# Performance work log

Measured on AMD Instinct MI355X. Metric: run time of the kernel, lower is better.

Reference implementation:

```python
import jax, jax.numpy as jnp
import numpy as np

MASK_VALUE = 0.0  # default `mask=0` scalar in the original forward


def setup_inputs() -> dict:
    key = jax.random.key(0)
    kq, kk, kv = jax.random.split(key, 3)
    b, n, d_k, d_v = 8, 2048, 64, 64
    q = jax.random.normal(kq, (b, n, d_k), dtype=jnp.float32)
    k = jax.random.normal(kk, (b, n, d_k), dtype=jnp.float32)
    v = jax.random.normal(kv, (b, n, d_v), dtype=jnp.float32)
    return {"q": q, "k": k, "v": v}


def reference(q, k, v):
    d_k = q.shape[-1]
    temper = jnp.asarray(d_k, q.dtype) ** 0.5
    # scores: (b, n, n)
    attn = jnp.einsum('bqd,bkd->bqk', q, k) / temper
    # equality-based masking: positions whose score exactly equals the
    # scalar `mask` (default 0) are set to -inf before softmax.
    attn = jnp.where(attn == MASK_VALUE, -jnp.inf, attn)
    # NOTE: the original code calls `attn.masked_fill(look_ahead_mask==0, -inf)`
    # WITHOUT assignment, so the look-ahead mask is a no-op; we omit it faithfully.
    attn = jax.nn.softmax(attn, axis=-1)
    out = jnp.einsum('bqk,bkd->bqd', attn, v)  # (b, n, d_v)
    return out
```

## Files before the change

kernel.cpp:

```cpp
#include <hip/hip_runtime.h>
#include <hip/hip_bf16.h>

typedef __bf16 bf16_t;
typedef bf16_t bf16x2 __attribute__((ext_vector_type(2)));
typedef bf16_t bf16x8 __attribute__((ext_vector_type(8)));
typedef float  floatx4  __attribute__((ext_vector_type(4)));
typedef float  floatx16 __attribute__((ext_vector_type(16)));
typedef int    intx2    __attribute__((ext_vector_type(2)));

constexpr int B = 8, N = 2048, D = 64;

__global__ __launch_bounds__(256)
void prepass_kernel(const float* __restrict__ k, const float* __restrict__ v,
                    bf16_t* __restrict__ kf, bf16_t* __restrict__ vf) {
    __shared__ float t[32 * 65];
    const int tid = threadIdx.x;
    const int b   = blockIdx.x & 7;
    const int kvb = blockIdx.x >> 3;
    const size_t inoff  = ((size_t)b * N + kvb * 32) * D;
    const size_t outoff = (size_t)(b * 64 + kvb) * 2048;

    {
        const float* src = k + inoff;
        floatx4 f0 = *(const floatx4*)(src + tid * 8);
        floatx4 f1 = *(const floatx4*)(src + tid * 8 + 4);
        bf16x8 o;
        #pragma unroll
        for (int j = 0; j < 4; ++j) { o[j] = (bf16_t)f0[j]; o[j + 4] = (bf16_t)f1[j]; }
        const int rr = tid >> 3, kd = (tid >> 1) & 3, hh = tid & 1;
        *(bf16x8*)(kf + outoff + (size_t)kd * 512 + (hh * 32 + rr) * 8) = o;
    }
    {
        const float* src = v + inoff;
        floatx4 f0 = *(const floatx4*)(src + tid * 8);
        floatx4 f1 = *(const floatx4*)(src + tid * 8 + 4);
        const int rr = tid >> 3, cc = (tid & 7) * 8;
        #pragma unroll
        for (int j = 0; j < 4; ++j) { t[rr * 65 + cc + j] = f0[j]; t[rr * 65 + cc + 4 + j] = f1[j]; }
        __syncthreads();
        const int s2 = tid >> 7, dblk = (tid >> 6) & 1, lane = tid & 63;
        const int hh = lane >> 5, l31 = lane & 31;
        bf16x8 o;
        #pragma unroll
        for (int j = 0; j < 8; ++j)
            o[j] = (bf16_t)t[(s2 * 16 + hh * 8 + j) * 65 + dblk * 32 + l31];
        *(bf16x8*)(vf + outoff + (size_t)(s2 * 2 + dblk) * 512 + lane * 8) = o;
    }
}

__global__ __launch_bounds__(512, 2)
void attn_kernel(const float* __restrict__ q, const bf16_t* __restrict__ kf,
                 const bf16_t* __restrict__ vf, float* __restrict__ out) {
    __shared__ float o_buf[8 * 2048];

    const int tid  = threadIdx.x;
    const int lane = tid & 63;
    const int cg   = tid >> 6;
    const int h    = lane >> 5;
    const int l31  = lane & 31;

    const int b  = blockIdx.x & 7;
    const int q0 = (blockIdx.x >> 3) * 64;

    const bf16_t* kfb = kf + (size_t)b * 131072;
    const bf16_t* vfb = vf + (size_t)b * 131072;

    constexpr float QSCALE = 0.125f * 1.4426950408889634f;
    bf16x8 qf[2][4];
    #pragma unroll
    for (int t = 0; t < 2; ++t) {
        const float* qp = q + ((size_t)b * N + q0 + t * 32 + l31) * D + h * 8;
        #pragma unroll
        for (int kd = 0; kd < 4; ++kd) {
            floatx4 f0 = *(const floatx4*)(qp + kd * 16);
            floatx4 f1 = *(const floatx4*)(qp + kd * 16 + 4);
            bf16x8 tt;
            #pragma unroll
            for (int j = 0; j < 4; ++j) {
                tt[j]     = (bf16_t)(f0[j] * QSCALE);
                tt[j + 4] = (bf16_t)(f1[j] * QSCALE);
            }
            qf[t][kd] = tt;
        }
    }

    floatx16 o_acc[2][2];
    #pragma unroll
    for (int t = 0; t < 2; ++t)
        #pragma unroll
        for (int d = 0; d < 2; ++d)
            #pragma unroll
            for (int i = 0; i < 16; ++i) o_acc[t][d][i] = 0.f;
    float l_run[2][2] = {{0.f, 0.f}, {0.f, 0.f}};

    bf16x8 kreg[4];
    #pragma unroll
    for (int kd = 0; kd < 4; ++kd)
        kreg[kd] = *(const bf16x8*)(kfb + (size_t)cg * 2048 + kd * 512 + lane * 8);

    #pragma unroll 2
    for (int it = 0; it < 8; ++it) {
        const size_t base = (size_t)(it * 8 + cg) * 2048;

        bf16x8 vreg[4];
        #pragma unroll
        for (int u = 0; u < 4; ++u)
            vreg[u] = *(const bf16x8*)(vfb + base + (size_t)u * 512 + lane * 8);

        floatx16 s[2];
        #pragma unroll
        for (int t = 0; t < 2; ++t)
            #pragma unroll
            for (int i = 0; i < 16; ++i) s[t][i] = 0.f;
        __builtin_amdgcn_s_setprio(1);
        #pragma unroll
        for (int kd = 0; kd < 4; ++kd)
            s[0] = __builtin_amdgcn_mfma_f32_32x32x16_bf16(kreg[kd], qf[0][kd], s[0], 0, 0, 0);
        #pragma unroll
        for (int kd = 0; kd < 4; ++kd)
            s[1] = __builtin_amdgcn_mfma_f32_32x32x16_bf16(kreg[kd], qf[1][kd], s[1], 0, 0, 0);
        __builtin_amdgcn_s_setprio(0);

        if (it + 1 < 8) {
            const size_t nbase = (size_t)((it + 1) * 8 + cg) * 2048;
            #pragma unroll
            for (int kd = 0; kd < 4; ++kd)
                kreg[kd] = *(const bf16x8*)(kfb + nbase + (size_t)kd * 512 + lane * 8);
        }

        #pragma unroll
        for (int t = 0; t < 2; ++t) {
            int q8[8];
            #pragma unroll
            for (int g = 0; g < 8; ++g) {
                union { int i; bf16x2 h2; } u;
                {
                    float x = s[t][2 * g + 0];
                    float p = (x == 0.0f) ? 0.0f : __builtin_amdgcn_exp2f(x);
                    l_run[t][0] += p;
                    u.h2[0] = (bf16_t)p;
                }
                {
                    float x = s[t][2 * g + 1];
                    float p = (x == 0.0f) ? 0.0f : __builtin_amdgcn_exp2f(x);
                    l_run[t][1] += p;
                    u.h2[1] = (bf16_t)p;
                }
                q8[g] = u.i;
            }

            #pragma unroll
            for (int s2 = 0; s2 < 2; ++s2) {
                intx2 p02 = __builtin_amdgcn_permlane32_swap(q8[4 * s2 + 0], q8[4 * s2 + 2], false, false);
                intx2 p13 = __builtin_amdgcn_permlane32_swap(q8[4 * s2 + 1], q8[4 * s2 + 3], false, false);
                union { int i4[4]; bf16x8 v; } bf;
                bf.i4[0] = p02[0];
                bf.i4[1] = p13[0];
                bf.i4[2] = p02[1];
                bf.i4[3] = p13[1];
                __builtin_amdgcn_s_setprio(1);
                #pragma unroll
                for (int dblk = 0; dblk < 2; ++dblk)
                    o_acc[t][dblk] = __builtin_amdgcn_mfma_f32_32x32x16_bf16(vreg[s2 * 2 + dblk], bf.v,
                                                                             o_acc[t][dblk], 0, 0, 0);
                __builtin_amdgcn_s_setprio(0);
            }
        }
    }

    #pragma unroll
    for (int t = 0; t < 2; ++t) {
        float l = l_run[t][0] + l_run[t][1];
        l += __shfl_xor(l, 32);
        l_run[t][0] = l;
    }

    if (h == 0) {
        o_buf[cg * 32 + l31]       = l_run[0][0];
        o_buf[256 + cg * 32 + l31] = l_run[1][0];
    }
    __syncthreads();
    float inv_l[2];
    {
        float s0 = 0.f, s1 = 0.f;
        #pragma unroll
        for (int w = 0; w < 8; ++w) {
            s0 += o_buf[w * 32 + l31];
            s1 += o_buf[256 + w * 32 + l31];
        }
        inv_l[0] = 1.0f / s0;
        inv_l[1] = 1.0f / s1;
    }

    #pragma unroll
    for (int t = 0; t < 2; ++t) {
        __syncthreads();
        {
            float* ob = o_buf + cg * 2048;
            #pragma unroll
            for (int dblk = 0; dblk < 2; ++dblk)
                #pragma unroll
                for (int i = 0; i < 16; ++i) {
                    const int d = (i & 3) + 8 * (i >> 2) + 4 * h + dblk * 32;
                    ob[d * 32 + l31] = o_acc[t][dblk][i];
                }
        }
        __syncthreads();
        {
            const int mdblk = cg >> 2, g = cg & 3;
            const int d0 = 8 * g + 4 * h + mdblk * 32;
            float* op = out + ((size_t)b * N + q0 + t * 32 + l31) * D;
            floatx4 o4;
            #pragma unroll
            for (int j = 0; j < 4; ++j) {
                float sum = 0.f;
                #pragma unroll
                for (int w = 0; w < 8; ++w)
                    sum += o_buf[w * 2048 + (d0 + j) * 32 + l31];
                o4[j] = sum * inv_l[t];
            }
            *(floatx4*)(op + d0) = o4;
        }
    }
}

extern "C" void kernel_launch(void* const* d_in, const int* in_sizes, int n_in,
                              void* d_out, int out_size, void* d_ws, size_t ws_size,
                              hipStream_t stream) {
    const float* q = (const float*)d_in[0];
    const float* k = (const float*)d_in[1];
    const float* v = (const float*)d_in[2];
    float* out = (float*)d_out;
    bf16_t* kfrag = (bf16_t*)d_ws;
    bf16_t* vfrag = (bf16_t*)((char*)d_ws + (size_t)B * N * D * 2);

    hipLaunchKernelGGL(prepass_kernel, dim3(512), dim3(256), 0, stream, k, v, kfrag, vfrag);
    hipLaunchKernelGGL(attn_kernel, dim3(256), dim3(512), 0, stream, q, kfrag, vfrag, out);
}
```

Baseline: 82.43 us.

## Fuse K/V bf16 conversion into attention kernel, drop prepass launch

Removes the separate prepass that converted K and V to bf16 fragment layout in a workspace, and instead loads fp32 K and V directly inside the attention kernel, converting to bf16 in registers. This saves one kernel launch and the workspace write/read round trip. The cost is that each of the 32 query-block CTAs per batch now re-reads and re-converts the fp32 K/V, which doubles the bytes fetched. V is loaded with strided scalar accesses, eight rows apart, instead of vectorized fragment loads.

```diff
diff --git a/kernel.cpp b/kernel.cpp
--- a/kernel.cpp
+++ b/kernel.cpp
@@ -10,47 +10,9 @@
 
 constexpr int B = 8, N = 2048, D = 64;
 
-__global__ __launch_bounds__(256)
-void prepass_kernel(const float* __restrict__ k, const float* __restrict__ v,
-                    bf16_t* __restrict__ kf, bf16_t* __restrict__ vf) {
-    __shared__ float t[32 * 65];
-    const int tid = threadIdx.x;
-    const int b   = blockIdx.x & 7;
-    const int kvb = blockIdx.x >> 3;
-    const size_t inoff  = ((size_t)b * N + kvb * 32) * D;
-    const size_t outoff = (size_t)(b * 64 + kvb) * 2048;
-
-    {
-        const float* src = k + inoff;
-        floatx4 f0 = *(const floatx4*)(src + tid * 8);
-        floatx4 f1 = *(const floatx4*)(src + tid * 8 + 4);
-        bf16x8 o;
-        #pragma unroll
-        for (int j = 0; j < 4; ++j) { o[j] = (bf16_t)f0[j]; o[j + 4] = (bf16_t)f1[j]; }
-        const int rr = tid >> 3, kd = (tid >> 1) & 3, hh = tid & 1;
-        *(bf16x8*)(kf + outoff + (size_t)kd * 512 + (hh * 32 + rr) * 8) = o;
-    }
-    {
-        const float* src = v + inoff;
-        floatx4 f0 = *(const floatx4*)(src + tid * 8);
-        floatx4 f1 = *(const floatx4*)(src + tid * 8 + 4);
-        const int rr = tid >> 3, cc = (tid & 7) * 8;
-        #pragma unroll
-        for (int j = 0; j < 4; ++j) { t[rr * 65 + cc + j] = f0[j]; t[rr * 65 + cc + 4 + j] = f1[j]; }
-        __syncthreads();
-        const int s2 = tid >> 7, dblk = (tid >> 6) & 1, lane = tid & 63;
-        const int hh = lane >> 5, l31 = lane & 31;
-        bf16x8 o;
-        #pragma unroll
-        for (int j = 0; j < 8; ++j)
-            o[j] = (bf16_t)t[(s2 * 16 + hh * 8 + j) * 65 + dblk * 32 + l31];
-        *(bf16x8*)(vf + outoff + (size_t)(s2 * 2 + dblk) * 512 + lane * 8) = o;
-    }
-}
-
 __global__ __launch_bounds__(512, 2)
-void attn_kernel(const float* __restrict__ q, const bf16_t* __restrict__ kf,
-                 const bf16_t* __restrict__ vf, float* __restrict__ out) {
+void attn_fused_kernel(const float* __restrict__ q, const float* __restrict__ k,
+                       const float* __restrict__ v, float* __restrict__ out) {
     __shared__ float o_buf[8 * 2048];
 
     const int tid  = threadIdx.x;
@@ -62,8 +24,8 @@
     const int b  = blockIdx.x & 7;
     const int q0 = (blockIdx.x >> 3) * 64;
 
-    const bf16_t* kfb = kf + (size_t)b * 131072;
-    const bf16_t* vfb = vf + (size_t)b * 131072;
+    const float* kb = k + (size_t)b * N * D;
+    const float* vb = v + (size_t)b * N * D;
 
     constexpr float QSCALE = 0.125f * 1.4426950408889634f;
     bf16x8 qf[2][4];
@@ -93,19 +55,37 @@
             for (int i = 0; i < 16; ++i) o_acc[t][d][i] = 0.f;
     float l_run[2][2] = {{0.f, 0.f}, {0.f, 0.f}};
 
+    auto load_k = [&](int kvb, bf16x8* kreg) {
+        const float* kp = kb + ((size_t)(kvb * 32) + l31) * D + h * 8;
+        #pragma unroll
+        for (int kd = 0; kd < 4; ++kd) {
+            floatx4 f0 = *(const floatx4*)(kp + kd * 16);
+            floatx4 f1 = *(const floatx4*)(kp + kd * 16 + 4);
+            bf16x8 o;
+            #pragma unroll
+            for (int j = 0; j < 4; ++j) { o[j] = (bf16_t)f0[j]; o[j + 4] = (bf16_t)f1[j]; }
+            kreg[kd] = o;
+        }
+    };
+
     bf16x8 kreg[4];
-    #pragma unroll
-    for (int kd = 0; kd < 4; ++kd)
-        kreg[kd] = *(const bf16x8*)(kfb + (size_t)cg * 2048 + kd * 512 + lane * 8);
+    load_k(cg, kreg);
 
     #pragma unroll 2
     for (int it = 0; it < 8; ++it) {
-        const size_t base = (size_t)(it * 8 + cg) * 2048;
+        const int kvb = it * 8 + cg;
 
         bf16x8 vreg[4];
         #pragma unroll
-        for (int u = 0; u < 4; ++u)
-            vreg[u] = *(const bf16x8*)(vfb + base + (size_t)u * 512 + lane * 8);
+        for (int s2 = 0; s2 < 2; ++s2)
+            #pragma unroll
+            for (int dblk = 0; dblk < 2; ++dblk) {
+                const float* vp = vb + ((size_t)(kvb * 32 + s2 * 16 + h * 8)) * D + dblk * 32 + l31;
+                bf16x8 o;
+                #pragma unroll
+                for (int j = 0; j < 8; ++j) o[j] = (bf16_t)vp[(size_t)j * D];
+                vreg[s2 * 2 + dblk] = o;
+            }
 
         floatx16 s[2];
         #pragma unroll
@@ -121,12 +101,7 @@
             s[1] = __builtin_amdgcn_mfma_f32_32x32x16_bf16(kreg[kd], qf[1][kd], s[1], 0, 0, 0);
         __builtin_amdgcn_s_setprio(0);
 
-        if (it + 1 < 8) {
-            const size_t nbase = (size_t)((it + 1) * 8 + cg) * 2048;
-            #pragma unroll
-            for (int kd = 0; kd < 4; ++kd)
-                kreg[kd] = *(const bf16x8*)(kfb + nbase + (size_t)kd * 512 + lane * 8);
-        }
+        if (it + 1 < 8) load_k((it + 1) * 8 + cg, kreg);
 
         #pragma unroll
         for (int t = 0; t < 2; ++t) {
@@ -231,9 +206,7 @@
     const float* k = (const float*)d_in[1];
     const float* v = (const float*)d_in[2];
     float* out = (float*)d_out;
-    bf16_t* kfrag = (bf16_t*)d_ws;
-    bf16_t* vfrag = (bf16_t*)((char*)d_ws + (size_t)B * N * D * 2);
-
-    hipLaunchKernelGGL(prepass_kernel, dim3(512), dim3(256), 0, stream, k, v, kfrag, vfrag);
-    hipLaunchKernelGGL(attn_kernel, dim3(256), dim3(512), 0, stream, q, kfrag, vfrag, out);
+    (void)d_ws; (void)ws_size;
+
+    hipLaunchKernelGGL(attn_fused_kernel, dim3(256), dim3(512), 0, stream, q, k, v, out);
 }
```

Measured after the change: 87.83 us. +6.6%, slower.
